# Optimization experiments

Measured on AMD Instinct MI355X. Metric: run time of the kernel, lower is better.

The kernel has to match this reference:

```python
import jax, jax.numpy as jnp
import numpy as np

B, N, D, H = 8, 1024, 768, 12
HD = D // H  # head_dim = 64
SCALE = HD ** (-0.5)


def setup_inputs() -> dict:
    key = jax.random.key(0)
    k1, k2, k3 = jax.random.split(key, 3)
    x = jax.random.normal(k1, (B, N, D), dtype=jnp.float32)
    w_qkv = jax.random.normal(k2, (D, 3 * D), dtype=jnp.float32) * (D ** -0.5)
    b_qkv = jnp.zeros((3 * D,), dtype=jnp.float32)
    w_proj = jax.random.normal(k3, (D, D), dtype=jnp.float32) * (D ** -0.5)
    b_proj = jnp.zeros((D,), dtype=jnp.float32)
    return {"x": x, "w_qkv": w_qkv, "b_qkv": b_qkv, "w_proj": w_proj, "b_proj": b_proj}


def reference(x, w_qkv, b_qkv, w_proj, b_proj):
    bsz, n, d = x.shape
    qkv = x @ w_qkv + b_qkv                         # [B, N, 3D]
    qkv = qkv.reshape(bsz, n, 3, H, HD)
    qkv = jnp.transpose(qkv, (2, 0, 3, 1, 4))       # [3, B, H, N, HD]
    q, k, v = qkv[0], qkv[1], qkv[2]
    attn = jnp.einsum('bhqd,bhkd->bhqk', q, k) * SCALE  # [B, H, N, N]
    attn = jax.nn.softmax(attn, axis=-1)
    out = jnp.einsum('bhqk,bhkd->bhqd', attn, v)    # [B, H, N, HD]
    out = jnp.transpose(out, (0, 2, 1, 3)).reshape(bsz, n, d)
    return out @ w_proj + b_proj
```

## Files before the change

kernel.cpp:

```cpp
#include <hip/hip_runtime.h>
#include <hip/hip_bf16.h>


typedef short bf16x8 __attribute__((ext_vector_type(8)));
typedef short bf16x4 __attribute__((ext_vector_type(4)));
typedef float f32x4 __attribute__((ext_vector_type(4)));

#define QSCALE 0.18033688011112042f

#define WAIT_VM(N) asm volatile("s_waitcnt vmcnt(" #N ")" ::: "memory")

__device__ inline short f2bf(float f) {
    __hip_bfloat16 h = __float2bfloat16(f);
    return __builtin_bit_cast(short, h);
}

__device__ inline unsigned cvtpk(float a, float b) {
    unsigned r;
    asm("v_cvt_pk_bf16_f32 %0, %1, %2" : "=v"(r) : "v"(a), "v"(b));
    return r;
}

__device__ inline f32x4 mfma16(bf16x4 a, bf16x4 b, f32x4 c) {
    return __builtin_amdgcn_mfma_f32_16x16x16bf16_1k(a, b, c, 0, 0, 0);
}

#define BKB 128
__device__ inline int swz(int row, int byte_in_row) {
    return (row * BKB + byte_in_row) ^ ((row & 7) << 4);
}

__device__ inline void gload_lds16(const void* g, void* l) {
    __builtin_amdgcn_global_load_lds(
        (const __attribute__((address_space(1))) unsigned int*)g,
        (__attribute__((address_space(3))) unsigned int*)l, 16, 0, 0);
}

__device__ inline void stage_tile(const __hip_bfloat16* __restrict__ gA,
                                  const __hip_bfloat16* __restrict__ gB,
                                  char* As, char* Bs, int wid, int sr, int sc16) {
#pragma unroll
    for (int j = 0; j < 4; ++j) {
        int slotbase = (wid * 4 + j) * 64;
        int r = (slotbase >> 3) + sr;
        gload_lds16(gA + (size_t)r * 768 + sc16 * 8, As + slotbase * 16);
        gload_lds16(gB + (size_t)r * 768 + sc16 * 8, Bs + slotbase * 16);
    }
}

__device__ inline void gemm_step(const char* As, const char* Bs, f32x4 acc[4][4],
                                 int wr, int wc, int lh, int lq) {
#pragma unroll
    for (int kki = 0; kki < 2; ++kki) {
        int kk = kki * 32;
        bf16x8 a[4], b[4];
#pragma unroll
        for (int mi = 0; mi < 4; ++mi)
            a[mi] = *(const bf16x8*)(As + swz(wr * 64 + mi * 16 + lh, (kk + lq * 8) * 2));
#pragma unroll
        for (int ni = 0; ni < 4; ++ni)
            b[ni] = *(const bf16x8*)(Bs + swz(wc * 64 + ni * 16 + lh, (kk + lq * 8) * 2));
#pragma unroll
        for (int mi = 0; mi < 4; ++mi)
#pragma unroll
            for (int ni = 0; ni < 4; ++ni)
                acc[mi][ni] = __builtin_amdgcn_mfma_f32_16x16x32_bf16(a[mi], b[ni], acc[mi][ni], 0, 0, 0);
    }
}

__device__ inline void transpose_body(const float* __restrict__ src,
                                      __hip_bfloat16* __restrict__ dst,
                                      int R, int C, int bx, int by,
                                      float (*tile)[33]) {
    int c0 = bx * 32, r0 = by * 32;
    int tx = threadIdx.x & 31, ty = threadIdx.x >> 5;
#pragma unroll
    for (int i = 0; i < 32; i += 8)
        tile[ty + i][tx] = src[(size_t)(r0 + ty + i) * C + c0 + tx];
    __syncthreads();
#pragma unroll
    for (int i = 0; i < 32; i += 8)
        dst[(size_t)(c0 + ty + i) * R + r0 + tx] = __float2bfloat16(tile[tx][ty + i]);
}

__global__ __launch_bounds__(256) void prep(const float* __restrict__ x,
                                            const float* __restrict__ w_qkv,
                                            const float* __restrict__ w_proj,
                                            __hip_bfloat16* __restrict__ Xb,
                                            __hip_bfloat16* __restrict__ wqt,
                                            __hip_bfloat16* __restrict__ wpt) {
    __shared__ float tile[32][33];
    const int bid = blockIdx.x;
    if (bid < 1728) {
        transpose_body(w_qkv, wqt, 768, 2304, bid % 72, bid / 72, tile);
    } else if (bid < 2304) {
        int b2 = bid - 1728;
        transpose_body(w_proj, wpt, 768, 768, b2 % 24, b2 / 24, tile);
    } else {
        int b3 = bid - 2304;
        const int n8 = 8192 * 768 / 8;
        for (int i = b3 * 256 + threadIdx.x; i < n8; i += 768 * 256) {
            float4 a = ((const float4*)x)[i * 2];
            float4 b = ((const float4*)x)[i * 2 + 1];
            union { short s[8]; uint4 v; } u;
            u.s[0] = f2bf(a.x); u.s[1] = f2bf(a.y); u.s[2] = f2bf(a.z); u.s[3] = f2bf(a.w);
            u.s[4] = f2bf(b.x); u.s[5] = f2bf(b.y); u.s[6] = f2bf(b.z); u.s[7] = f2bf(b.w);
            ((uint4*)Xb)[i] = u.v;
        }
    }
}

__global__ __launch_bounds__(256) void qkv_gemm(const __hip_bfloat16* __restrict__ Xb,
                                                const __hip_bfloat16* __restrict__ Wt,
                                                const float* __restrict__ bias,
                                                __hip_bfloat16* __restrict__ Qo,
                                                __hip_bfloat16* __restrict__ Ko,
                                                __hip_bfloat16* __restrict__ Vto) {
    __shared__ __align__(16) char As0[16384], Bs0[16384], As1[16384], Bs1[16384];
    char* Asb[2] = {As0, As1};
    char* Bsb[2] = {Bs0, Bs1};
    const int orig = blockIdx.y * 18 + blockIdx.x;
    const int swzid = (orig & 7) * 144 + (orig >> 3);
    const int m0 = (swzid / 18) * 128;
    const int n0 = (swzid % 18) * 128;
    const int tid = threadIdx.x;
    const int lane = tid & 63, wid = tid >> 6;
    const int wr = wid >> 1, wc = wid & 1;
    const int lh = lane & 15, lq = lane >> 4;
    const int sr = lane >> 3;
    const int sc16 = (lane & 7) ^ (sr & 7);

    const __hip_bfloat16* gA = Xb + (size_t)m0 * 768;
    const __hip_bfloat16* gB = Wt + (size_t)n0 * 768;

    f32x4 acc[4][4] = {};

    stage_tile(gA, gB, As0, Bs0, wid, sr, sc16);
#pragma unroll
    for (int t = 0; t < 12; ++t) {
        if (t < 11) {
            stage_tile(gA + (t + 1) * 64, gB + (t + 1) * 64,
                       Asb[(t + 1) & 1], Bsb[(t + 1) & 1], wid, sr, sc16);
            WAIT_VM(8);
        } else {
            WAIT_VM(0);
        }
        __builtin_amdgcn_sched_barrier(0);
        __builtin_amdgcn_s_barrier();
        gemm_step(Asb[t & 1], Bsb[t & 1], acc, wr, wc, lh, lq);
        __builtin_amdgcn_s_barrier();
    }

#pragma unroll
    for (int ni = 0; ni < 4; ++ni) {
        int col = n0 + wc * 64 + ni * 16 + lh;
        float bv = bias[col];
        int which = col / 768;
        int rem = col - which * 768;
        int h = rem >> 6, hd = rem & 63;
        if (which == 2) {
#pragma unroll
            for (int mi = 0; mi < 4; ++mi) {
                int row0 = m0 + wr * 64 + mi * 16 + lq * 4;
                int bb = row0 >> 10, rr0 = row0 & 1023;
                int head = bb * 12 + h;
                bf16x4 pk;
#pragma unroll
                for (int j = 0; j < 4; ++j) pk[j] = f2bf(acc[mi][ni][j] + bv);
                *(bf16x4*)(Vto + ((size_t)head * 64 + hd) * 1024 + rr0) = pk;
            }
        } else {
            const float sc = (which == 0) ? QSCALE : 1.f;
            __hip_bfloat16* dst = (which == 0) ? Qo : Ko;
#pragma unroll
            for (int mi = 0; mi < 4; ++mi) {
#pragma unroll
                for (int j = 0; j < 4; ++j) {
                    int row = m0 + wr * 64 + mi * 16 + lq * 4 + j;
                    int bb = row >> 10, rr = row & 1023;
                    int head = bb * 12 + h;
                    dst[((size_t)head * 1024 + rr) * 64 + hd] =
                        __float2bfloat16((acc[mi][ni][j] + bv) * sc);
                }
            }
        }
    }
}

__global__ __launch_bounds__(256, 3) void attn_kernel(const __hip_bfloat16* __restrict__ Q,
                                                      const __hip_bfloat16* __restrict__ K,
                                                      const __hip_bfloat16* __restrict__ Vt,
                                                      __hip_bfloat16* __restrict__ Ao) {
    __shared__ __align__(16) char kvlds[2 * 16384];
    const int head = blockIdx.x;
    const int qt = blockIdx.y;
    const int tid = threadIdx.x;
    const int lane = tid & 63, w = tid >> 6;
    const int lh = lane & 15, lq = lane >> 4;
    const int q0 = qt * 128 + w * 32;
    const size_t hoff = (size_t)head * 65536;
    const __hip_bfloat16* Kg = K + hoff;
    const __hip_bfloat16* Vg = Vt + hoff;
    const int sr = lane >> 3;
    const int sc16 = (lane & 7) ^ (sr & 7);

    const int mfield = (lh & 7) << 4;
    const int rowb = lh * 128;
    const int kb0 = (lq * 16) ^ mfield;
    const int kb1 = (64 | (lq * 16)) ^ mfield;
    int vb[4];
#pragma unroll
    for (int kf = 0; kf < 4; ++kf) vb[kf] = ((kf * 32) | (lq * 8)) ^ mfield;

    const bf16x4 ONES = {0x3F80, 0x3F80, 0x3F80, 0x3F80};

    bf16x8 qf[2][2];
#pragma unroll
    for (int qi = 0; qi < 2; ++qi)
#pragma unroll
        for (int kki = 0; kki < 2; ++kki)
            qf[qi][kki] = *(const bf16x8*)(Q + hoff + (size_t)(q0 + qi * 16 + lh) * 64 + kki * 32 + lq * 8);

    f32x4 accT[2][4] = {};
    f32x4 accL[2] = {};

    const __hip_bfloat16* kg0 = Kg + (size_t)((w * 2) * 8 + sr) * 64 + sc16 * 8;
    const __hip_bfloat16* kg1 = kg0 + 8 * 64;
    const __hip_bfloat16* vg0 = Vg + (size_t)((w * 2) * 8 + sr) * 1024 + sc16 * 8;
    const __hip_bfloat16* vg1 = vg0 + 8 * 1024;
    const int kd = (w * 2) * 1024;

    gload_lds16(kg0, kvlds + kd);
    gload_lds16(kg1, kvlds + kd + 1024);
    gload_lds16(vg0, kvlds + 8192 + kd);
    gload_lds16(vg1, kvlds + 8192 + kd + 1024);
    kg0 += 4096; kg1 += 4096; vg0 += 64; vg1 += 64;
    __syncthreads();

    auto step = [&](int kt, char* Ks, char* Vs, char* Kn) {
        if (kt < 15) {
            gload_lds16(kg0, Kn + kd);
            gload_lds16(kg1, Kn + kd + 1024);
            gload_lds16(vg0, Kn + 8192 + kd);
            gload_lds16(vg1, Kn + 8192 + kd + 1024);
            kg0 += 4096; kg1 += 4096; vg0 += 64; vg1 += 64;
        }
        f32x4 sT[2][4] = {};
        __builtin_amdgcn_s_setprio(1);
#pragma unroll
        for (int kf = 0; kf < 4; ++kf) {
            bf16x8 k0v = *(const bf16x8*)(Ks + rowb + kf * 2048 + kb0);
            sT[0][kf] = __builtin_amdgcn_mfma_f32_16x16x32_bf16(k0v, qf[0][0], sT[0][kf], 0, 0, 0);
            sT[1][kf] = __builtin_amdgcn_mfma_f32_16x16x32_bf16(k0v, qf[1][0], sT[1][kf], 0, 0, 0);
            bf16x8 k1v = *(const bf16x8*)(Ks + rowb + kf * 2048 + kb1);
            sT[0][kf] = __builtin_amdgcn_mfma_f32_16x16x32_bf16(k1v, qf[0][1], sT[0][kf], 0, 0, 0);
            sT[1][kf] = __builtin_amdgcn_mfma_f32_16x16x32_bf16(k1v, qf[1][1], sT[1][kf], 0, 0, 0);
        }
        __builtin_amdgcn_s_setprio(0);
        bf16x4 pb[2][4];
#pragma unroll
        for (int qi = 0; qi < 2; ++qi) {
#pragma unroll
            for (int kf = 0; kf < 4; ++kf) {
                float p0 = __builtin_amdgcn_exp2f(sT[qi][kf][0]);
                float p1 = __builtin_amdgcn_exp2f(sT[qi][kf][1]);
                float p2 = __builtin_amdgcn_exp2f(sT[qi][kf][2]);
                float p3 = __builtin_amdgcn_exp2f(sT[qi][kf][3]);
                union { unsigned u[2]; bf16x4 v; } uu;
                uu.u[0] = cvtpk(p0, p1);
                uu.u[1] = cvtpk(p2, p3);
                pb[qi][kf] = uu.v;
            }
        }
        __builtin_amdgcn_s_setprio(1);
#pragma unroll
        for (int kf = 0; kf < 4; ++kf) {
            accL[0] = mfma16(ONES, pb[0][kf], accL[0]);
            accL[1] = mfma16(ONES, pb[1][kf], accL[1]);
#pragma unroll
            for (int hf = 0; hf < 4; ++hf) {
                bf16x4 vfr = *(const bf16x4*)(Vs + rowb + hf * 2048 + vb[kf]);
                accT[0][hf] = mfma16(vfr, pb[0][kf], accT[0][hf]);
                accT[1][hf] = mfma16(vfr, pb[1][kf], accT[1][hf]);
            }
        }
        __builtin_amdgcn_s_setprio(0);
        __syncthreads();
    };

#pragma unroll 1
    for (int kt2 = 0; kt2 < 16; kt2 += 2) {
        step(kt2, kvlds, kvlds + 8192, kvlds + 16384);
        step(kt2 + 1, kvlds + 16384, kvlds + 16384 + 8192, kvlds);
    }

    const int b = head / 12, h = head - (head / 12) * 12;
#pragma unroll
    for (int qi = 0; qi < 2; ++qi) {
        float inv = 1.f / accL[qi][0];
        int q = q0 + qi * 16 + lh;
#pragma unroll
        for (int hf = 0; hf < 4; ++hf) {
            bf16x4 pk;
#pragma unroll
            for (int j = 0; j < 4; ++j) pk[j] = f2bf(accT[qi][hf][j] * inv);
            *(bf16x4*)(Ao + ((size_t)(b * 1024 + q)) * 768 + h * 64 + hf * 16 + lq * 4) = pk;
        }
    }
}

__global__ __launch_bounds__(256) void proj_gemm(const __hip_bfloat16* __restrict__ A,
                                                 const __hip_bfloat16* __restrict__ Wt,
                                                 const float* __restrict__ bias,
                                                 float* __restrict__ Out) {
    __shared__ __align__(16) char As0[16384], Bs0[16384], As1[16384], Bs1[16384];
    char* Asb[2] = {As0, As1};
    char* Bsb[2] = {Bs0, Bs1};
    const int orig = blockIdx.y * 6 + blockIdx.x;
    const int swzid = (orig & 7) * 48 + (orig >> 3);
    const int m0 = (swzid / 6) * 128;
    const int n0 = (swzid % 6) * 128;
    const int tid = threadIdx.x;
    const int lane = tid & 63, wid = tid >> 6;
    const int wr = wid >> 1, wc = wid & 1;
    const int lh = lane & 15, lq = lane >> 4;
    const int sr = lane >> 3;
    const int sc16 = (lane & 7) ^ (sr & 7);

    const __hip_bfloat16* gA = A + (size_t)m0 * 768;
    const __hip_bfloat16* gB = Wt + (size_t)n0 * 768;

    f32x4 acc[4][4] = {};

    stage_tile(gA, gB, As0, Bs0, wid, sr, sc16);
#pragma unroll
    for (int t = 0; t < 12; ++t) {
        if (t < 11) {
            stage_tile(gA + (t + 1) * 64, gB + (t + 1) * 64,
                       Asb[(t + 1) & 1], Bsb[(t + 1) & 1], wid, sr, sc16);
            WAIT_VM(8);
        } else {
            WAIT_VM(0);
        }
        __builtin_amdgcn_sched_barrier(0);
        __builtin_amdgcn_s_barrier();
        gemm_step(Asb[t & 1], Bsb[t & 1], acc, wr, wc, lh, lq);
        __builtin_amdgcn_s_barrier();
    }

#pragma unroll
    for (int ni = 0; ni < 4; ++ni) {
        int col = n0 + wc * 64 + ni * 16 + lh;
        float bv = bias[col];
#pragma unroll
        for (int mi = 0; mi < 4; ++mi) {
#pragma unroll
            for (int j = 0; j < 4; ++j) {
                int row = m0 + wr * 64 + mi * 16 + lq * 4 + j;
                Out[(size_t)row * 768 + col] = acc[mi][ni][j] + bv;
            }
        }
    }
}

extern "C" void kernel_launch(void* const* d_in, const int* in_sizes, int n_in,
                              void* d_out, int out_size, void* d_ws, size_t ws_size,
                              hipStream_t stream) {
    const float* x      = (const float*)d_in[0];
    const float* w_qkv  = (const float*)d_in[1];
    const float* b_qkv  = (const float*)d_in[2];
    const float* w_proj = (const float*)d_in[3];
    const float* b_proj = (const float*)d_in[4];
    float* out = (float*)d_out;

    __hip_bfloat16* ws = (__hip_bfloat16*)d_ws;
    __hip_bfloat16* wqt = ws;
    __hip_bfloat16* wpt = wqt + 2304 * 768;
    __hip_bfloat16* Qb  = wpt + 768 * 768;
    __hip_bfloat16* Kb  = Qb + 96 * 1024 * 64;
    __hip_bfloat16* Vt  = Kb + 96 * 1024 * 64;
    __hip_bfloat16* Ao  = Vt + 96 * 1024 * 64;
    __hip_bfloat16* Xb  = Ao + 8192 * 768;

    prep<<<3072, 256, 0, stream>>>(x, w_qkv, w_proj, Xb, wqt, wpt);
    qkv_gemm<<<dim3(18, 64), 256, 0, stream>>>(Xb, wqt, b_qkv, Qb, Kb, Vt);
    attn_kernel<<<dim3(96, 8), 256, 0, stream>>>(Qb, Kb, Vt, Ao);
    proj_gemm<<<dim3(6, 64), 256, 0, stream>>>(Ao, wpt, b_proj, out);
}
```

Measured before the change: 100.7 us.

## Use 8-wave GEMM blocks with 64x32 warp tiles and syncthreads double buffering

Both GEMM kernels go from 256 to 512 threads per block. Each wave now computes a 64x32 sub-tile, so per-wave accumulators and B-fragment loads are halved and more waves share each 128x128 tile. The pipeline drops the explicit vmcnt waits and sched barriers in favour of __syncthreads ping-pong over the two LDS buffers. This should raise latency hiding per CU, but it relies on __syncthreads implying vmcnt(0) for the async LDS loads, which serialises prefetch against compute and adds barrier cost.

```diff
diff --git a/kernel.cpp b/kernel.cpp
--- a/kernel.cpp
+++ b/kernel.cpp
@@ -7,8 +7,6 @@
 typedef float f32x4 __attribute__((ext_vector_type(4)));
 
 #define QSCALE 0.18033688011112042f
-
-#define WAIT_VM(N) asm volatile("s_waitcnt vmcnt(" #N ")" ::: "memory")
 
 __device__ inline short f2bf(float f) {
     __hip_bfloat16 h = __float2bfloat16(f);
@@ -36,34 +34,34 @@
         (__attribute__((address_space(3))) unsigned int*)l, 16, 0, 0);
 }
 
-__device__ inline void stage_tile(const __hip_bfloat16* __restrict__ gA,
-                                  const __hip_bfloat16* __restrict__ gB,
-                                  char* As, char* Bs, int wid, int sr, int sc16) {
-#pragma unroll
-    for (int j = 0; j < 4; ++j) {
-        int slotbase = (wid * 4 + j) * 64;
+__device__ inline void stage_tile8(const __hip_bfloat16* __restrict__ gA,
+                                   const __hip_bfloat16* __restrict__ gB,
+                                   char* As, char* Bs, int wid, int sr, int sc16) {
+#pragma unroll
+    for (int j = 0; j < 2; ++j) {
+        int slotbase = (wid * 2 + j) * 64;
         int r = (slotbase >> 3) + sr;
         gload_lds16(gA + (size_t)r * 768 + sc16 * 8, As + slotbase * 16);
         gload_lds16(gB + (size_t)r * 768 + sc16 * 8, Bs + slotbase * 16);
     }
 }
 
-__device__ inline void gemm_step(const char* As, const char* Bs, f32x4 acc[4][4],
-                                 int wr, int wc, int lh, int lq) {
+__device__ inline void gemm_step8(const char* As, const char* Bs, f32x4 acc[4][2],
+                                  int wr, int wc, int lh, int lq) {
 #pragma unroll
     for (int kki = 0; kki < 2; ++kki) {
         int kk = kki * 32;
-        bf16x8 a[4], b[4];
+        bf16x8 a[4], b[2];
 #pragma unroll
         for (int mi = 0; mi < 4; ++mi)
             a[mi] = *(const bf16x8*)(As + swz(wr * 64 + mi * 16 + lh, (kk + lq * 8) * 2));
 #pragma unroll
-        for (int ni = 0; ni < 4; ++ni)
-            b[ni] = *(const bf16x8*)(Bs + swz(wc * 64 + ni * 16 + lh, (kk + lq * 8) * 2));
+        for (int ni = 0; ni < 2; ++ni)
+            b[ni] = *(const bf16x8*)(Bs + swz(wc * 32 + ni * 16 + lh, (kk + lq * 8) * 2));
 #pragma unroll
         for (int mi = 0; mi < 4; ++mi)
 #pragma unroll
-            for (int ni = 0; ni < 4; ++ni)
+            for (int ni = 0; ni < 2; ++ni)
                 acc[mi][ni] = __builtin_amdgcn_mfma_f32_16x16x32_bf16(a[mi], b[ni], acc[mi][ni], 0, 0, 0);
     }
 }
@@ -110,22 +108,20 @@
     }
 }
 
-__global__ __launch_bounds__(256) void qkv_gemm(const __hip_bfloat16* __restrict__ Xb,
+__global__ __launch_bounds__(512) void qkv_gemm(const __hip_bfloat16* __restrict__ Xb,
                                                 const __hip_bfloat16* __restrict__ Wt,
                                                 const float* __restrict__ bias,
                                                 __hip_bfloat16* __restrict__ Qo,
                                                 __hip_bfloat16* __restrict__ Ko,
                                                 __hip_bfloat16* __restrict__ Vto) {
     __shared__ __align__(16) char As0[16384], Bs0[16384], As1[16384], Bs1[16384];
-    char* Asb[2] = {As0, As1};
-    char* Bsb[2] = {Bs0, Bs1};
     const int orig = blockIdx.y * 18 + blockIdx.x;
     const int swzid = (orig & 7) * 144 + (orig >> 3);
     const int m0 = (swzid / 18) * 128;
     const int n0 = (swzid % 18) * 128;
     const int tid = threadIdx.x;
     const int lane = tid & 63, wid = tid >> 6;
-    const int wr = wid >> 1, wc = wid & 1;
+    const int wr = wid >> 2, wc = wid & 3;
     const int lh = lane & 15, lq = lane >> 4;
     const int sr = lane >> 3;
     const int sc16 = (lane & 7) ^ (sr & 7);
@@ -133,27 +129,24 @@
     const __hip_bfloat16* gA = Xb + (size_t)m0 * 768;
     const __hip_bfloat16* gB = Wt + (size_t)n0 * 768;
 
-    f32x4 acc[4][4] = {};
-
-    stage_tile(gA, gB, As0, Bs0, wid, sr, sc16);
-#pragma unroll
-    for (int t = 0; t < 12; ++t) {
-        if (t < 11) {
-            stage_tile(gA + (t + 1) * 64, gB + (t + 1) * 64,
-                       Asb[(t + 1) & 1], Bsb[(t + 1) & 1], wid, sr, sc16);
-            WAIT_VM(8);
-        } else {
-            WAIT_VM(0);
-        }
-        __builtin_amdgcn_sched_barrier(0);
-        __builtin_amdgcn_s_barrier();
-        gemm_step(Asb[t & 1], Bsb[t & 1], acc, wr, wc, lh, lq);
-        __builtin_amdgcn_s_barrier();
-    }
-
-#pragma unroll
-    for (int ni = 0; ni < 4; ++ni) {
-        int col = n0 + wc * 64 + ni * 16 + lh;
+    f32x4 acc[4][2] = {};
+
+    stage_tile8(gA, gB, As0, Bs0, wid, sr, sc16);
+    __syncthreads();
+#pragma unroll
+    for (int t = 0; t < 12; t += 2) {
+        stage_tile8(gA + (t + 1) * 64, gB + (t + 1) * 64, As1, Bs1, wid, sr, sc16);
+        gemm_step8(As0, Bs0, acc, wr, wc, lh, lq);
+        __syncthreads();
+        if (t + 2 < 12)
+            stage_tile8(gA + (t + 2) * 64, gB + (t + 2) * 64, As0, Bs0, wid, sr, sc16);
+        gemm_step8(As1, Bs1, acc, wr, wc, lh, lq);
+        __syncthreads();
+    }
+
+#pragma unroll
+    for (int ni = 0; ni < 2; ++ni) {
+        int col = n0 + wc * 32 + ni * 16 + lh;
         float bv = bias[col];
         int which = col / 768;
         int rem = col - which * 768;
@@ -309,20 +302,18 @@
     }
 }
 
-__global__ __launch_bounds__(256) void proj_gemm(const __hip_bfloat16* __restrict__ A,
+__global__ __launch_bounds__(512) void proj_gemm(const __hip_bfloat16* __restrict__ A,
                                                  const __hip_bfloat16* __restrict__ Wt,
                                                  const float* __restrict__ bias,
                                                  float* __restrict__ Out) {
     __shared__ __align__(16) char As0[16384], Bs0[16384], As1[16384], Bs1[16384];
-    char* Asb[2] = {As0, As1};
-    char* Bsb[2] = {Bs0, Bs1};
     const int orig = blockIdx.y * 6 + blockIdx.x;
     const int swzid = (orig & 7) * 48 + (orig >> 3);
     const int m0 = (swzid / 6) * 128;
     const int n0 = (swzid % 6) * 128;
     const int tid = threadIdx.x;
     const int lane = tid & 63, wid = tid >> 6;
-    const int wr = wid >> 1, wc = wid & 1;
+    const int wr = wid >> 2, wc = wid & 3;
     const int lh = lane & 15, lq = lane >> 4;
     const int sr = lane >> 3;
     const int sc16 = (lane & 7) ^ (sr & 7);
@@ -330,27 +321,24 @@
     const __hip_bfloat16* gA = A + (size_t)m0 * 768;
     const __hip_bfloat16* gB = Wt + (size_t)n0 * 768;
 
-    f32x4 acc[4][4] = {};
-
-    stage_tile(gA, gB, As0, Bs0, wid, sr, sc16);
-#pragma unroll
-    for (int t = 0; t < 12; ++t) {
-        if (t < 11) {
-            stage_tile(gA + (t + 1) * 64, gB + (t + 1) * 64,
-                       Asb[(t + 1) & 1], Bsb[(t + 1) & 1], wid, sr, sc16);
-            WAIT_VM(8);
-        } else {
-            WAIT_VM(0);
-        }
-        __builtin_amdgcn_sched_barrier(0);
-        __builtin_amdgcn_s_barrier();
-        gemm_step(Asb[t & 1], Bsb[t & 1], acc, wr, wc, lh, lq);
-        __builtin_amdgcn_s_barrier();
-    }
-
-#pragma unroll
-    for (int ni = 0; ni < 4; ++ni) {
-        int col = n0 + wc * 64 + ni * 16 + lh;
+    f32x4 acc[4][2] = {};
+
+    stage_tile8(gA, gB, As0, Bs0, wid, sr, sc16);
+    __syncthreads();
+#pragma unroll
+    for (int t = 0; t < 12; t += 2) {
+        stage_tile8(gA + (t + 1) * 64, gB + (t + 1) * 64, As1, Bs1, wid, sr, sc16);
+        gemm_step8(As0, Bs0, acc, wr, wc, lh, lq);
+        __syncthreads();
+        if (t + 2 < 12)
+            stage_tile8(gA + (t + 2) * 64, gB + (t + 2) * 64, As0, Bs0, wid, sr, sc16);
+        gemm_step8(As1, Bs1, acc, wr, wc, lh, lq);
+        __syncthreads();
+    }
+
+#pragma unroll
+    for (int ni = 0; ni < 2; ++ni) {
+        int col = n0 + wc * 32 + ni * 16 + lh;
         float bv = bias[col];
 #pragma unroll
         for (int mi = 0; mi < 4; ++mi) {
@@ -383,7 +371,7 @@
     __hip_bfloat16* Xb  = Ao + 8192 * 768;
 
     prep<<<3072, 256, 0, stream>>>(x, w_qkv, w_proj, Xb, wqt, wpt);
-    qkv_gemm<<<dim3(18, 64), 256, 0, stream>>>(Xb, wqt, b_qkv, Qb, Kb, Vt);
+    qkv_gemm<<<dim3(18, 64), 512, 0, stream>>>(Xb, wqt, b_qkv, Qb, Kb, Vt);
     attn_kernel<<<dim3(96, 8), 256, 0, stream>>>(Qb, Kb, Vt, Ao);
-    proj_gemm<<<dim3(6, 64), 256, 0, stream>>>(Ao, wpt, b_proj, out);
-}
+    proj_gemm<<<dim3(6, 64), 512, 0, stream>>>(Ao, wpt, b_proj, out);
+}
```

Result: slower. 108.7 us (+7.9%).
